# Optimization experiments

Measured on AMD Instinct MI355X. Metric: run time of the kernel, lower is better.

The kernel has to match this reference:

```python
import jax, jax.numpy as jnp
import numpy as np

IN_CH = 1024
OUT_CH = 1024
BATCH = 4096


def setup_inputs() -> dict:
    key = jax.random.key(0)
    ks = jax.random.split(key, 8)
    s = 1.0 / np.sqrt(IN_CH)
    return {
        "hidden_rep": jax.random.normal(ks[0], (1, BATCH, IN_CH), jnp.float32),
        "W_ih": jax.random.uniform(ks[1], (3 * IN_CH, IN_CH), jnp.float32, -s, s),
        "W_hh": jax.random.uniform(ks[2], (3 * IN_CH, IN_CH), jnp.float32, -s, s),
        "b_ih": jax.random.uniform(ks[3], (3 * IN_CH,), jnp.float32, -s, s),
        "b_hh": jax.random.uniform(ks[4], (3 * IN_CH,), jnp.float32, -s, s),
        "W_out": jax.random.uniform(ks[5], (OUT_CH, IN_CH), jnp.float32, -s, s),
        "b_out": jax.random.uniform(ks[6], (OUT_CH,), jnp.float32, -s, s),
        "max_try": 16,
    }


def _gru_cell(x, h, W_ih, W_hh, b_ih, b_hh):
    # x, h: (B, H). PyTorch GRU gate ordering: reset, update, new.
    gi = x @ W_ih.T + b_ih  # (B, 3H)
    gh = h @ W_hh.T + b_hh  # (B, 3H)
    i_r, i_z, i_n = jnp.split(gi, 3, axis=-1)
    h_r, h_z, h_n = jnp.split(gh, 3, axis=-1)
    r = jax.nn.sigmoid(i_r + h_r)
    z = jax.nn.sigmoid(i_z + h_z)
    n = jnp.tanh(i_n + r * h_n)
    return (1.0 - z) * n + z * h


def reference(hidden_rep, W_ih, W_hh, b_ih, b_hh, W_out, b_out, max_try):
    h0 = hidden_rep[0]           # (B, H) initial hidden state
    x0 = jnp.zeros_like(h0)      # zeros_like(hidden_rep): first input is zeros

    def step(carry, _):
        x, h = carry
        h_new = _gru_cell(x, h, W_ih, W_hh, b_ih, b_hh)
        # seq output of single-layer GRU == new hidden; it is fed back as next input
        out = jax.nn.relu(h_new) @ W_out.T + b_out
        return (h_new, h_new), out

    _, outs = jax.lax.scan(step, (x0, h0), None, length=max_try)
    return outs  # (max_try, B, OUT_CH) == torch.cat(outputs, dim=0)
```

## Files before the change

kernel.cpp:

```cpp
#include <hip/hip_runtime.h>
#include <hip/hip_bf16.h>


#define H_DIM 1024
#define BATCH_N 4096
#define NSTEPS 16
#define K4 (4 * H_DIM)

typedef __bf16 bf16_t;
typedef __bf16 bf16x8 __attribute__((ext_vector_type(8)));
typedef float f32x4 __attribute__((ext_vector_type(4)));

__device__ __forceinline__ float sigm(float x) { return 1.0f / (1.0f + __expf(-x)); }


__global__ __launch_bounds__(256) void prep_weights(
    const float* __restrict__ Wih, const float* __restrict__ Whh,
    const float* __restrict__ bih, const float* __restrict__ bhh,
    const float* __restrict__ Wout,
    bf16_t* __restrict__ Wc0, bf16_t* __restrict__ Wc,
    bf16_t* __restrict__ Wob, float* __restrict__ biasc)
{
    const int stride = gridDim.x * blockDim.x;
    const int idx = blockIdx.x * blockDim.x + threadIdx.x;

    const int total = K4 * H_DIM;
    for (int i = idx; i < total; i += stride) {
        const int c2 = i >> 10;
        const int col = i & (H_DIM - 1);
        const int gate = (c2 >> 4) & 3;
        const int hc = ((c2 >> 6) << 4) | (c2 & 15);
        float vc, v0;
        if (gate == 0) {
            float a = Wih[(size_t)hc * H_DIM + col];
            float b = Whh[(size_t)hc * H_DIM + col];
            vc = a + b; v0 = b;
        } else if (gate == 1) {
            float a = Wih[(size_t)(H_DIM + hc) * H_DIM + col];
            float b = Whh[(size_t)(H_DIM + hc) * H_DIM + col];
            vc = a + b; v0 = b;
        } else if (gate == 2) {
            vc = Wih[(size_t)(2 * H_DIM + hc) * H_DIM + col];
            v0 = 0.0f;
        } else {
            float b = Whh[(size_t)(2 * H_DIM + hc) * H_DIM + col];
            vc = b; v0 = b;
        }
        Wc[i]  = (bf16_t)vc;
        Wc0[i] = (bf16_t)v0;
    }
    for (int i = idx; i < H_DIM * H_DIM; i += stride)
        Wob[i] = (bf16_t)Wout[i];
    for (int i = idx; i < K4; i += stride) {
        const int gate = i >> 10;
        const int hc = i & (H_DIM - 1);
        float v;
        if (gate == 0)      v = bih[hc] + bhh[hc];
        else if (gate == 1) v = bih[H_DIM + hc] + bhh[H_DIM + hc];
        else if (gate == 2) v = bih[2 * H_DIM + hc];
        else                v = bhh[2 * H_DIM + hc];
        biasc[i] = v;
    }
}

__global__ __launch_bounds__(256) void prep_h(
    const float* __restrict__ h0, bf16_t* __restrict__ hb)
{
    const int stride = gridDim.x * blockDim.x;
    for (int i = blockIdx.x * blockDim.x + threadIdx.x; i < BATCH_N * H_DIM; i += stride)
        hb[i] = (bf16_t)h0[i];
}


__device__ __forceinline__ void stage_half(
    const bf16_t* __restrict__ g, int grow0, int K, int k0,
    bf16_t* ldsbase, int l)
{
    const int colsrc = (((l & 3) ^ ((l >> 3) & 3)) << 3);
    const bf16_t* ga = g + (size_t)(grow0 + (l >> 2)) * K + k0 + colsrc;
    __builtin_amdgcn_global_load_lds(
        (const __attribute__((address_space(1))) void*)ga,
        (__attribute__((address_space(3))) void*)ldsbase, 16, 0, 0);
}

template <bool FUSED>
__global__ __launch_bounds__(512, 2) void gemm256(
    const bf16_t* __restrict__ A, const bf16_t* __restrict__ Bm,
    int M, int N, int K,
    float* __restrict__ C, const float* __restrict__ bias,
    const float* __restrict__ biasc,
    bf16_t* __restrict__ hbout, bf16_t* __restrict__ hr)
{
    __shared__ bf16_t lds[65536];

    const int tid = threadIdx.x;
    const int l = tid & 63;
    const int w = tid >> 6;
    const int wr = w >> 2;
    const int wc = w & 3;

    int bx, by;
    if constexpr (FUSED) {
        const int d = blockIdx.x;
        const int r = d & 7, s = d >> 3;
        bx = (r & 3) * 4 + (s & 3);
        by = (r >> 2) * 8 + (s >> 2);
    } else {
        const int nbx = N >> 8;
        const int cpx = gridDim.x >> 3;
        const int d = blockIdx.x;
        const int bid = (d & 7) * cpx + (d >> 3);
        bx = bid % nbx;
        by = bid / nbx;
    }
    const int brow = by * 256;
    const int bcol = bx * 256;

    bf16_t* ldsA = lds;
    bf16_t* ldsB = lds + 32768;

    f32x4 acc[8][4];
    const f32x4 zero = {0.f, 0.f, 0.f, 0.f};
#pragma unroll
    for (int m = 0; m < 8; ++m)
#pragma unroll
        for (int n = 0; n < 4; ++n) acc[m][n] = zero;

    const int nk = K >> 5;

#define STAGE_A(u, half)  stage_half(A,  brow + (half) * 128 + w * 16, K, (u) * 32, \
        ldsA + ((u) & 3) * 8192 + ((half) * 128 + w * 16) * 32, l)
#define STAGE_B(u, half)  stage_half(Bm, bcol + (half) * 128 + w * 16, K, (u) * 32, \
        ldsB + ((u) & 3) * 8192 + ((half) * 128 + w * 16) * 32, l)

    for (int u = 0; u < 3 && u < nk; ++u) {
        STAGE_A(u, 0); STAGE_A(u, 1);
        STAGE_B(u, 0); STAGE_B(u, 1);
    }

    const int colrd = (((l >> 4) ^ ((l >> 1) & 3)) << 3);
    const int ar0 = (wr * 128 + (l & 15)) * 32 + colrd;
    const int br0 = (wc * 64 + (l & 15)) * 32 + colrd;

    for (int t = 0; t < nk; ++t) {
        const int rem = nk - 1 - t;
        if (rem >= 2)      asm volatile("s_waitcnt vmcnt(8)" ::: "memory");
        else if (rem == 1) asm volatile("s_waitcnt vmcnt(4)" ::: "memory");
        else               asm volatile("s_waitcnt vmcnt(0)" ::: "memory");
        __builtin_amdgcn_s_barrier();

        const int pu = t + 3;
        const int ab = (t & 3) * 8192;
        bf16x8 bfrag[4], afrag[4];

        if (pu < nk) { STAGE_A(pu, 0); STAGE_A(pu, 1); }
#pragma unroll
        for (int n = 0; n < 4; ++n)
            bfrag[n] = *(const bf16x8*)&ldsB[ab + br0 + n * 512];
#pragma unroll
        for (int m = 0; m < 4; ++m)
            afrag[m] = *(const bf16x8*)&ldsA[ab + ar0 + m * 512];
        __builtin_amdgcn_s_setprio(1);
#pragma unroll
        for (int m = 0; m < 4; ++m)
#pragma unroll
            for (int n = 0; n < 4; ++n)
                acc[m][n] = __builtin_amdgcn_mfma_f32_16x16x32_bf16(afrag[m], bfrag[n], acc[m][n], 0, 0, 0);
        __builtin_amdgcn_s_setprio(0);
        __builtin_amdgcn_s_barrier();

        if (pu < nk) { STAGE_B(pu, 0); STAGE_B(pu, 1); }
#pragma unroll
        for (int m = 0; m < 4; ++m)
            afrag[m] = *(const bf16x8*)&ldsA[ab + ar0 + (m + 4) * 512];
        __builtin_amdgcn_s_setprio(1);
#pragma unroll
        for (int m = 0; m < 4; ++m)
#pragma unroll
            for (int n = 0; n < 4; ++n)
                acc[m + 4][n] = __builtin_amdgcn_mfma_f32_16x16x32_bf16(afrag[m], bfrag[n], acc[m + 4][n], 0, 0, 0);
        __builtin_amdgcn_s_setprio(0);
    }
#undef STAGE_A
#undef STAGE_B

    if constexpr (FUSED) {
        const int hc = (bx * 4 + wc) * 16 + (l & 15);
        const float br_ = biasc[hc];
        const float bz_ = biasc[H_DIM + hc];
        const float bi_ = biasc[2 * H_DIM + hc];
        const float bh_ = biasc[3 * H_DIM + hc];
        const int r0 = brow + wr * 128 + ((l >> 4) << 2);
#pragma unroll
        for (int m = 0; m < 8; ++m) {
#pragma unroll
            for (int j = 0; j < 4; ++j) {
                const int row = r0 + m * 16 + j;
                const size_t o = (size_t)row * H_DIM + hc;
                const float hold = (float)A[o];
                const float r = sigm(acc[m][0][j] + br_);
                const float z = sigm(acc[m][1][j] + bz_);
                float a = acc[m][2][j] + bi_ + r * (acc[m][3][j] + bh_);
                a = fminf(fmaxf(a, -30.f), 30.f);
                const float e = __expf(-2.f * a);
                const float nn = (1.f - e) / (1.f + e);
                const float hn = (1.f - z) * nn + z * hold;
                hbout[o] = (bf16_t)hn;
                hr[o] = (bf16_t)fmaxf(hn, 0.f);
            }
        }
    } else {
        const int r0 = brow + wr * 128 + ((l >> 4) << 2);
        const int c0 = bcol + wc * 64 + (l & 15);
#pragma unroll
        for (int m = 0; m < 8; ++m) {
#pragma unroll
            for (int n = 0; n < 4; ++n) {
                const int col = c0 + n * 16;
                const float badd = bias ? bias[col] : 0.0f;
#pragma unroll
                for (int j = 0; j < 4; ++j) {
                    const int row = r0 + m * 16 + j;
                    C[(size_t)row * N + col] = acc[m][n][j] + badd;
                }
            }
        }
    }
}


extern "C" void kernel_launch(void* const* d_in, const int* in_sizes, int n_in,
                              void* d_out, int out_size, void* d_ws, size_t ws_size,
                              hipStream_t stream)
{
    const float* hidden = (const float*)d_in[0];
    const float* Wih = (const float*)d_in[1];
    const float* Whh = (const float*)d_in[2];
    const float* bih = (const float*)d_in[3];
    const float* bhh = (const float*)d_in[4];
    const float* Wout = (const float*)d_in[5];
    const float* bout = (const float*)d_in[6];
    float* out = (float*)d_out;
    (void)in_sizes; (void)n_in; (void)out_size;

    char* ws = (char*)d_ws;
    size_t off = 0;
    bf16_t* Wc0 = (bf16_t*)(ws + off); off += (size_t)K4 * H_DIM * 2;
    bf16_t* Wc  = (bf16_t*)(ws + off); off += (size_t)K4 * H_DIM * 2;
    bf16_t* Wob = (bf16_t*)(ws + off); off += (size_t)H_DIM * H_DIM * 2;
    float*  biasc = (float*)(ws + off); off += (size_t)K4 * 4;
    bf16_t* hbA = (bf16_t*)(ws + off); off += (size_t)BATCH_N * H_DIM * 2;
    bf16_t* hbB = (bf16_t*)(ws + off); off += (size_t)BATCH_N * H_DIM * 2;

    const size_t hr_step = (size_t)BATCH_N * H_DIM;
    const size_t need_batched = off + NSTEPS * hr_step * 2;
    const bool batched = (ws_size >= need_batched);
    bf16_t* hr_all = (bf16_t*)(ws + off);

    prep_weights<<<1024, 256, 0, stream>>>(Wih, Whh, bih, bhh, Wout, Wc0, Wc, Wob, biasc);
    prep_h<<<2048, 256, 0, stream>>>(hidden, hbA);

    for (int t = 0; t < NSTEPS; ++t) {
        bf16_t* hin  = (t & 1) ? hbB : hbA;
        bf16_t* hout = (t & 1) ? hbA : hbB;
        bf16_t* hr_t = batched ? (hr_all + (size_t)t * hr_step) : hr_all;
        gemm256<true><<<(BATCH_N / 256) * (K4 / 256), 512, 0, stream>>>(
            hin, (t == 0) ? Wc0 : Wc, BATCH_N, K4, H_DIM,
            nullptr, nullptr, biasc, hout, hr_t);
        if (!batched) {
            gemm256<false><<<(BATCH_N / 256) * (H_DIM / 256), 512, 0, stream>>>(
                hr_t, Wob, BATCH_N, H_DIM, H_DIM,
                out + (size_t)t * hr_step, bout, nullptr, nullptr, nullptr);
        }
    }
    if (batched) {
        gemm256<false><<<((NSTEPS * BATCH_N) / 256) * (H_DIM / 256), 512, 0, stream>>>(
            hr_all, Wob, NSTEPS * BATCH_N, H_DIM, H_DIM,
            out, bout, nullptr, nullptr, nullptr);
    }
}
```

Baseline: 825.3 us.

## Restructure GEMM main loop pipeline with interleaved LDS stages and explicit barriers

```diff
diff --git a/kernel.cpp b/kernel.cpp
--- a/kernel.cpp
+++ b/kernel.cpp
@@ -116,9 +116,6 @@
     const int brow = by * 256;
     const int bcol = bx * 256;
 
-    bf16_t* ldsA = lds;
-    bf16_t* ldsB = lds + 32768;
-
     f32x4 acc[8][4];
     const f32x4 zero = {0.f, 0.f, 0.f, 0.f};
 #pragma unroll
@@ -126,40 +123,43 @@
 #pragma unroll
         for (int n = 0; n < 4; ++n) acc[m][n] = zero;
 
-    const int nk = K >> 5;
-
-#define STAGE_A(u, half)  stage_half(A,  brow + (half) * 128 + w * 16, K, (u) * 32, \
-        ldsA + ((u) & 3) * 8192 + ((half) * 128 + w * 16) * 32, l)
-#define STAGE_B(u, half)  stage_half(Bm, bcol + (half) * 128 + w * 16, K, (u) * 32, \
-        ldsB + ((u) & 3) * 8192 + ((half) * 128 + w * 16) * 32, l)
-
-    for (int u = 0; u < 3 && u < nk; ++u) {
-        STAGE_A(u, 0); STAGE_A(u, 1);
-        STAGE_B(u, 0); STAGE_B(u, 1);
-    }
+    const int Z = K >> 5;
+
+#define STAGE_A(zz) do { \
+    bf16_t* lb_ = lds + ((zz) & 3) * 16384 + w * 512; \
+    stage_half(A, brow + w * 16, K, (zz) * 32, lb_, l); \
+    stage_half(A, brow + 128 + w * 16, K, (zz) * 32, lb_ + 4096, l); \
+} while (0)
+#define STAGE_B(zz) do { \
+    bf16_t* lb_ = lds + ((zz) & 3) * 16384 + 8192 + w * 512; \
+    stage_half(Bm, bcol + w * 16, K, (zz) * 32, lb_, l); \
+    stage_half(Bm, bcol + 128 + w * 16, K, (zz) * 32, lb_ + 4096, l); \
+} while (0)
+
+    STAGE_A(0); STAGE_B(0);
+    STAGE_A(1); STAGE_B(1);
+    STAGE_A(2); STAGE_B(2);
+    asm volatile("s_waitcnt vmcnt(8)" ::: "memory");
+    __builtin_amdgcn_s_barrier();
 
     const int colrd = (((l >> 4) ^ ((l >> 1) & 3)) << 3);
     const int ar0 = (wr * 128 + (l & 15)) * 32 + colrd;
-    const int br0 = (wc * 64 + (l & 15)) * 32 + colrd;
-
-    for (int t = 0; t < nk; ++t) {
-        const int rem = nk - 1 - t;
-        if (rem >= 2)      asm volatile("s_waitcnt vmcnt(8)" ::: "memory");
-        else if (rem == 1) asm volatile("s_waitcnt vmcnt(4)" ::: "memory");
-        else               asm volatile("s_waitcnt vmcnt(0)" ::: "memory");
-        __builtin_amdgcn_s_barrier();
-
-        const int pu = t + 3;
-        const int ab = (t & 3) * 8192;
-        bf16x8 bfrag[4], afrag[4];
-
-        if (pu < nk) { STAGE_A(pu, 0); STAGE_A(pu, 1); }
+    const int br0 = 8192 + (wc * 64 + (l & 15)) * 32 + colrd;
+
+    bf16x8 afrag[4], bfrag[4];
+    for (int z = 0; z < Z; ++z) {
+        const int sb = (z & 3) * 16384;
+
 #pragma unroll
         for (int n = 0; n < 4; ++n)
-            bfrag[n] = *(const bf16x8*)&ldsB[ab + br0 + n * 512];
-#pragma unroll
-        for (int m = 0; m < 4; ++m)
-            afrag[m] = *(const bf16x8*)&ldsA[ab + ar0 + m * 512];
+            bfrag[n] = *(const bf16x8*)&lds[sb + br0 + n * 512];
+#pragma unroll
+        for (int m = 0; m < 4; ++m)
+            afrag[m] = *(const bf16x8*)&lds[sb + ar0 + m * 512];
+        if (z + 3 < Z) STAGE_A(z + 3);
+        __builtin_amdgcn_s_barrier();
+        asm volatile("s_waitcnt lgkmcnt(0)" ::: "memory");
+        __builtin_amdgcn_sched_barrier(0);
         __builtin_amdgcn_s_setprio(1);
 #pragma unroll
         for (int m = 0; m < 4; ++m)
@@ -169,10 +169,16 @@
         __builtin_amdgcn_s_setprio(0);
         __builtin_amdgcn_s_barrier();
 
-        if (pu < nk) { STAGE_B(pu, 0); STAGE_B(pu, 1); }
-#pragma unroll
-        for (int m = 0; m < 4; ++m)
-            afrag[m] = *(const bf16x8*)&ldsA[ab + ar0 + (m + 4) * 512];
+#pragma unroll
+        for (int m = 0; m < 4; ++m)
+            afrag[m] = *(const bf16x8*)&lds[sb + ar0 + (m + 4) * 512];
+        if (z + 3 < Z) STAGE_B(z + 3);
+        if (z < Z - 3)       asm volatile("s_waitcnt vmcnt(8)" ::: "memory");
+        else if (z == Z - 3) asm volatile("s_waitcnt vmcnt(4)" ::: "memory");
+        else                 asm volatile("s_waitcnt vmcnt(0)" ::: "memory");
+        __builtin_amdgcn_s_barrier();
+        asm volatile("s_waitcnt lgkmcnt(0)" ::: "memory");
+        __builtin_amdgcn_sched_barrier(0);
         __builtin_amdgcn_s_setprio(1);
 #pragma unroll
         for (int m = 0; m < 4; ++m)
@@ -180,6 +186,7 @@
             for (int n = 0; n < 4; ++n)
                 acc[m + 4][n] = __builtin_amdgcn_mfma_f32_16x16x32_bf16(afrag[m], bfrag[n], acc[m + 4][n], 0, 0, 0);
         __builtin_amdgcn_s_setprio(0);
+        __builtin_amdgcn_s_barrier();
     }
 #undef STAGE_A
 #undef STAGE_B
```

After: 835.6 us. About the same (+1.2%).
